# Kernel optimization log

Measured on AMD Instinct MI355X. Metric: run time of the kernel, lower is better.

The kernel has to match this reference:

```python
import jax, jax.numpy as jnp
import numpy as np


def setup_inputs() -> dict:
    key = jax.random.key(0)
    k1, k2 = jax.random.split(key)
    n, c, h, w = 4, 64, 128, 128
    x = jax.random.normal(k1, (n, c, h, w), dtype=jnp.float32)
    # weight holds 9 stencil taps per channel, layout matches F.unfold: (n, c*9, h, w)
    weight = jax.random.normal(k2, (n, c * 9, h, w), dtype=jnp.float32)
    return {"x": x, "weight": weight, "max_step": 8}


def reference(x, weight, max_step):
    n, c, h, w = x.shape
    # normalize |w| over the 9 taps (done once, outside the loop, as in the original)
    wgt = jnp.abs(weight.reshape(n, c, 9, h, w))
    wgt = wgt / jnp.sum(wgt, axis=2, keepdims=True)

    steps = min(max_step, max(h, w))  # static Python ints -> static trip count

    def step(xx, _):
        # 3x3 patches via 9 shifted views of the padded image; tap order k = ki*3 + kj
        # matches F.unfold's row-major kernel ordering.
        xp = jnp.pad(xx, ((0, 0), (0, 0), (1, 1), (1, 1)))
        patches = jnp.stack(
            [xp[:, :, i:i + h, j:j + w] for i in range(3) for j in range(3)],
            axis=2,
        )  # (n, c, 9, h, w)
        return jnp.sum(patches * wgt, axis=2), None

    x_out, _ = jax.lax.scan(step, x, None, length=steps)
    return x_out
```

## Files before the change

### kernel.cpp

```cpp
#include <hip/hip_runtime.h>
#include <hip/hip_fp16.h>


constexpr int H = 128, W = 128, PLANE = H * W;
constexpr int NSTEP = 8;
constexpr int RPT = 5;
constexpr int NRG = 16;
constexpr int HALO = 8;
constexpr int OWN = 64;

#define MKWIN(D, V) do {                                                     \
    (D)[1] = (V).x; (D)[2] = (V).y; (D)[3] = (V).z; (D)[4] = (V).w;          \
    float _l = __shfl_up((V).w, 1);                                          \
    float _r = __shfl_down((V).x, 1);                                        \
    (D)[0] = (quad == 0)  ? 0.f : _l;                                        \
    (D)[5] = (quad == 31) ? 0.f : _r;                                        \
} while (0)

__global__ __launch_bounds__(512)
void diff_fused(const float* __restrict__ xin,
                const float* __restrict__ wgt,
                float* __restrict__ out)
{
    __shared__ float ldsT[NRG][W];
    __shared__ float ldsB[NRG][W];
    __shared__ uint2 whL[9][512];

    const int tid   = threadIdx.x;
    const int quad  = tid & 31;
    const int rg    = tid >> 5;
    const int j0    = quad * 4;
    const int plane = blockIdx.x >> 1;
    const int half  = blockIdx.x & 1;
    const int rbase = half * OWN - HALO;
    const int r0    = rbase + rg * RPT;
    const size_t pbase = (size_t)plane * PLANE;

    const float* __restrict__ xp = xin + pbase;
    const float* __restrict__ wb = wgt + pbase * 9;

    __half2 wh[RPT - 1][9][2];
    #pragma unroll
    for (int p = 0; p < RPT; ++p) {
        const int  gr  = r0 + p;
        const bool inr = (unsigned)gr < (unsigned)H;
        const float* wr = wb + gr * W + j0;
        float a[9][4];
        float s0 = 0.f, s1 = 0.f, s2 = 0.f, s3 = 0.f;
        #pragma unroll
        for (int k = 0; k < 9; ++k) {
            float4 v = make_float4(1.f, 1.f, 1.f, 1.f);
            if (inr) v = *reinterpret_cast<const float4*>(wr + (size_t)k * PLANE);
            a[k][0] = fabsf(v.x); a[k][1] = fabsf(v.y);
            a[k][2] = fabsf(v.z); a[k][3] = fabsf(v.w);
            s0 += a[k][0]; s1 += a[k][1]; s2 += a[k][2]; s3 += a[k][3];
        }
        s0 = 1.f / s0; s1 = 1.f / s1; s2 = 1.f / s2; s3 = 1.f / s3;
        #pragma unroll
        for (int k = 0; k < 9; ++k) {
            __half2 h0 = __halves2half2(__float2half_rn(a[k][0] * s0),
                                        __float2half_rn(a[k][1] * s1));
            __half2 h1 = __halves2half2(__float2half_rn(a[k][2] * s2),
                                        __float2half_rn(a[k][3] * s3));
            if (p < RPT - 1) {
                wh[p][k][0] = h0;
                wh[p][k][1] = h1;
            } else {
                whL[k][tid] = make_uint2(__builtin_bit_cast(unsigned int, h0),
                                         __builtin_bit_cast(unsigned int, h1));
            }
        }
    }

    float4 xr[RPT];
    #pragma unroll
    for (int p = 0; p < RPT; ++p) {
        const int gr = r0 + p;
        xr[p] = make_float4(0.f, 0.f, 0.f, 0.f);
        if ((unsigned)gr < (unsigned)H)
            xr[p] = *reinterpret_cast<const float4*>(xp + gr * W + j0);
    }
    __syncthreads();

    #pragma unroll 1
    for (int s = 0; s < NSTEP; ++s) {
        *reinterpret_cast<float4*>(&ldsT[rg][j0]) = xr[0];
        *reinterpret_cast<float4*>(&ldsB[rg][j0]) = xr[RPT - 1];
        __syncthreads();
        float4 up = make_float4(0.f, 0.f, 0.f, 0.f);
        float4 dn = make_float4(0.f, 0.f, 0.f, 0.f);
        if (rg > 0)       up = *reinterpret_cast<const float4*>(&ldsB[rg - 1][j0]);
        if (rg < NRG - 1) dn = *reinterpret_cast<const float4*>(&ldsT[rg + 1][j0]);
        __syncthreads();

        float win[3][6];
        MKWIN(win[0], up);
        MKWIN(win[1], xr[0]);
        #pragma unroll
        for (int p = 0; p < RPT; ++p) {
            if (p < RPT - 1) { MKWIN(win[(p + 2) % 3], xr[p + 1]); }
            else             { MKWIN(win[(p + 2) % 3], dn); }
            float a0 = 0.f, a1 = 0.f, a2 = 0.f, a3 = 0.f;
            #pragma unroll
            for (int di = 0; di < 3; ++di) {
                #pragma unroll
                for (int dj = 0; dj < 3; ++dj) {
                    const int k = di * 3 + dj;
                    __half2 w0, w1;
                    if (p < RPT - 1) { w0 = wh[p][k][0]; w1 = wh[p][k][1]; }
                    else {
                        uint2 lv = whL[k][tid];
                        w0 = __builtin_bit_cast(__half2, lv.x);
                        w1 = __builtin_bit_cast(__half2, lv.y);
                    }
                    a0 = fmaf(__low2float (w0), win[(p + di) % 3][dj + 0], a0);
                    a1 = fmaf(__high2float(w0), win[(p + di) % 3][dj + 1], a1);
                    a2 = fmaf(__low2float (w1), win[(p + di) % 3][dj + 2], a2);
                    a3 = fmaf(__high2float(w1), win[(p + di) % 3][dj + 3], a3);
                }
            }
            xr[p] = make_float4(a0, a1, a2, a3);
        }
        #pragma unroll
        for (int p = 0; p < RPT; ++p) {
            const int gr = r0 + p;
            if ((unsigned)gr >= (unsigned)H)
                xr[p] = make_float4(0.f, 0.f, 0.f, 0.f);
        }
    }

    float* __restrict__ op = out + pbase;
    #pragma unroll
    for (int p = 0; p < RPT; ++p) {
        const int gr = r0 + p;
        const int lr = gr - half * OWN;
        if ((unsigned)lr < (unsigned)OWN)
            *reinterpret_cast<float4*>(op + gr * W + j0) = xr[p];
    }
}

extern "C" void kernel_launch(void* const* d_in, const int* in_sizes, int n_in,
                              void* d_out, int out_size, void* d_ws, size_t ws_size,
                              hipStream_t stream)
{
    const float* x = (const float*)d_in[0];
    const float* w = (const float*)d_in[1];
    float* out = (float*)d_out;
    (void)d_ws; (void)ws_size; (void)in_sizes; (void)n_in; (void)out_size;

    diff_fused<<<dim3(2 * 4 * 64), dim3(512), 0, stream>>>(x, w, out);
}
```

Baseline: 270.2 us.

## Split planes into quarter tiles with double-buffered halo exchange and register-only weights

Each plane is now split into four 32-row tiles with 3 rows per thread instead of two 64-row tiles with 5 rows per thread, which doubles the block count. Weights for every row now stay in registers (no LDS spill for the last row). A launch-bounds occupancy hint is added, and the halo exchange is double-buffered so each step needs one barrier instead of two. In exchange, the 8-row halo on each side now makes up a larger share of each tile, so more x and weight data is loaded and computed redundantly.

```diff
diff --git a/kernel.cpp b/kernel.cpp
--- a/kernel.cpp
+++ b/kernel.cpp
@@ -4,10 +4,10 @@
 
 constexpr int H = 128, W = 128, PLANE = H * W;
 constexpr int NSTEP = 8;
-constexpr int RPT = 5;
-constexpr int NRG = 16;
+constexpr int RPT  = 3;
+constexpr int NRG  = 16;
 constexpr int HALO = 8;
-constexpr int OWN = 64;
+constexpr int OWN  = 32;
 
 #define MKWIN(D, V) do {                                                     \
     (D)[1] = (V).x; (D)[2] = (V).y; (D)[3] = (V).z; (D)[4] = (V).w;          \
@@ -17,29 +17,28 @@
     (D)[5] = (quad == 31) ? 0.f : _r;                                        \
 } while (0)
 
-__global__ __launch_bounds__(512)
+__global__ __launch_bounds__(512, 4)
 void diff_fused(const float* __restrict__ xin,
                 const float* __restrict__ wgt,
                 float* __restrict__ out)
 {
-    __shared__ float ldsT[NRG][W];
-    __shared__ float ldsB[NRG][W];
-    __shared__ uint2 whL[9][512];
+    __shared__ float ldsT[2][NRG][W];
+    __shared__ float ldsB[2][NRG][W];
 
     const int tid   = threadIdx.x;
     const int quad  = tid & 31;
     const int rg    = tid >> 5;
     const int j0    = quad * 4;
-    const int plane = blockIdx.x >> 1;
-    const int half  = blockIdx.x & 1;
-    const int rbase = half * OWN - HALO;
+    const int plane = blockIdx.x >> 2;
+    const int qtr   = blockIdx.x & 3;
+    const int rbase = qtr * OWN - HALO;
     const int r0    = rbase + rg * RPT;
     const size_t pbase = (size_t)plane * PLANE;
 
     const float* __restrict__ xp = xin + pbase;
     const float* __restrict__ wb = wgt + pbase * 9;
 
-    __half2 wh[RPT - 1][9][2];
+    __half2 wh[RPT][9][2];
     #pragma unroll
     for (int p = 0; p < RPT; ++p) {
         const int  gr  = r0 + p;
@@ -58,17 +57,10 @@
         s0 = 1.f / s0; s1 = 1.f / s1; s2 = 1.f / s2; s3 = 1.f / s3;
         #pragma unroll
         for (int k = 0; k < 9; ++k) {
-            __half2 h0 = __halves2half2(__float2half_rn(a[k][0] * s0),
-                                        __float2half_rn(a[k][1] * s1));
-            __half2 h1 = __halves2half2(__float2half_rn(a[k][2] * s2),
-                                        __float2half_rn(a[k][3] * s3));
-            if (p < RPT - 1) {
-                wh[p][k][0] = h0;
-                wh[p][k][1] = h1;
-            } else {
-                whL[k][tid] = make_uint2(__builtin_bit_cast(unsigned int, h0),
-                                         __builtin_bit_cast(unsigned int, h1));
-            }
+            wh[p][k][0] = __halves2half2(__float2half_rn(a[k][0] * s0),
+                                         __float2half_rn(a[k][1] * s1));
+            wh[p][k][1] = __halves2half2(__float2half_rn(a[k][2] * s2),
+                                         __float2half_rn(a[k][3] * s3));
         }
     }
 
@@ -80,18 +72,18 @@
         if ((unsigned)gr < (unsigned)H)
             xr[p] = *reinterpret_cast<const float4*>(xp + gr * W + j0);
     }
+
+    *reinterpret_cast<float4*>(&ldsT[0][rg][j0]) = xr[0];
+    *reinterpret_cast<float4*>(&ldsB[0][rg][j0]) = xr[RPT - 1];
     __syncthreads();
 
     #pragma unroll 1
     for (int s = 0; s < NSTEP; ++s) {
-        *reinterpret_cast<float4*>(&ldsT[rg][j0]) = xr[0];
-        *reinterpret_cast<float4*>(&ldsB[rg][j0]) = xr[RPT - 1];
-        __syncthreads();
+        const int cur = s & 1;
         float4 up = make_float4(0.f, 0.f, 0.f, 0.f);
         float4 dn = make_float4(0.f, 0.f, 0.f, 0.f);
-        if (rg > 0)       up = *reinterpret_cast<const float4*>(&ldsB[rg - 1][j0]);
-        if (rg < NRG - 1) dn = *reinterpret_cast<const float4*>(&ldsT[rg + 1][j0]);
-        __syncthreads();
+        if (rg > 0)       up = *reinterpret_cast<const float4*>(&ldsB[cur][rg - 1][j0]);
+        if (rg < NRG - 1) dn = *reinterpret_cast<const float4*>(&ldsT[cur][rg + 1][j0]);
 
         float win[3][6];
         MKWIN(win[0], up);
@@ -106,13 +98,8 @@
                 #pragma unroll
                 for (int dj = 0; dj < 3; ++dj) {
                     const int k = di * 3 + dj;
-                    __half2 w0, w1;
-                    if (p < RPT - 1) { w0 = wh[p][k][0]; w1 = wh[p][k][1]; }
-                    else {
-                        uint2 lv = whL[k][tid];
-                        w0 = __builtin_bit_cast(__half2, lv.x);
-                        w1 = __builtin_bit_cast(__half2, lv.y);
-                    }
+                    const __half2 w0 = wh[p][k][0];
+                    const __half2 w1 = wh[p][k][1];
                     a0 = fmaf(__low2float (w0), win[(p + di) % 3][dj + 0], a0);
                     a1 = fmaf(__high2float(w0), win[(p + di) % 3][dj + 1], a1);
                     a2 = fmaf(__low2float (w1), win[(p + di) % 3][dj + 2], a2);
@@ -127,13 +114,18 @@
             if ((unsigned)gr >= (unsigned)H)
                 xr[p] = make_float4(0.f, 0.f, 0.f, 0.f);
         }
+        if (s < NSTEP - 1) {
+            *reinterpret_cast<float4*>(&ldsT[cur ^ 1][rg][j0]) = xr[0];
+            *reinterpret_cast<float4*>(&ldsB[cur ^ 1][rg][j0]) = xr[RPT - 1];
+            __syncthreads();
+        }
     }
 
     float* __restrict__ op = out + pbase;
     #pragma unroll
     for (int p = 0; p < RPT; ++p) {
         const int gr = r0 + p;
-        const int lr = gr - half * OWN;
+        const int lr = gr - rbase - HALO;
         if ((unsigned)lr < (unsigned)OWN)
             *reinterpret_cast<float4*>(op + gr * W + j0) = xr[p];
     }
@@ -148,5 +140,5 @@
     float* out = (float*)d_out;
     (void)d_ws; (void)ws_size; (void)in_sizes; (void)n_in; (void)out_size;
 
-    diff_fused<<<dim3(2 * 4 * 64), dim3(512), 0, stream>>>(x, w, out);
+    diff_fused<<<dim3(4 * 4 * 64), dim3(512), 0, stream>>>(x, w, out);
 }
```

New measurement: 388.0 us. +43.6%, slower.
